# Performance work log

Hardware: AMD Instinct MI355X
Metric: run time of the kernel (lower is better)

## Reference

```python
import jax, jax.numpy as jnp
import numpy as np

LATENT = 128
HEADS = 4
HEAD_DIM = LATENT // HEADS
NUM_BUCKETS = 32
MAX_DISTANCE = 100000
B, N = 8, 2048


def relative_position_bucket(qpos, kpos):
    """T5-style bidirectional relative position bucketing.
    qpos, kpos: [B, N] int -> buckets [B, N, N] int32 in [0, NUM_BUCKETS).
    """
    rel = kpos[:, None, :] - qpos[:, :, None]  # [B, Nq, Nk]
    half = NUM_BUCKETS // 2
    buckets = (rel > 0).astype(jnp.int32) * half
    arel = jnp.abs(rel)
    max_exact = half // 2
    is_small = arel < max_exact
    # log-spaced buckets for larger distances
    large = max_exact + (
        jnp.log(jnp.maximum(arel, 1).astype(jnp.float32) / max_exact)
        / np.log(MAX_DISTANCE / max_exact)
        * (half - max_exact)
    ).astype(jnp.int32)
    large = jnp.minimum(large, half - 1)
    return buckets + jnp.where(is_small, arel.astype(jnp.int32), large)


def setup_inputs() -> dict:
    key = jax.random.key(0)
    ks = jax.random.split(key, 12)
    s = 0.02
    x = jax.random.normal(ks[0], (B, N, LATENT), dtype=jnp.float32)
    positions = jnp.sort(jax.random.randint(ks[1], (B, N), 0, 1000000), axis=-1)
    mask = jnp.ones((B, N), dtype=bool)
    Wq = jax.random.normal(ks[2], (LATENT, LATENT), dtype=jnp.float32) * s
    bq = jax.random.normal(ks[3], (LATENT,), dtype=jnp.float32) * s
    Wk = jax.random.normal(ks[4], (LATENT, LATENT), dtype=jnp.float32) * s
    bk = jax.random.normal(ks[5], (LATENT,), dtype=jnp.float32) * s
    Wv = jax.random.normal(ks[6], (LATENT, LATENT), dtype=jnp.float32) * s
    bv = jax.random.normal(ks[7], (LATENT,), dtype=jnp.float32) * s
    pos_w = jax.random.normal(ks[8], (NUM_BUCKETS + 1, HEADS), dtype=jnp.float32) * s
    Wo = jax.random.normal(ks[9], (LATENT, LATENT), dtype=jnp.float32) * s
    bo = jax.random.normal(ks[10], (LATENT,), dtype=jnp.float32) * s
    return {"x": x, "positions": positions, "mask": mask,
            "Wq": Wq, "bq": bq, "Wk": Wk, "bk": bk, "Wv": Wv, "bv": bv,
            "pos_w": pos_w, "Wo": Wo, "bo": bo}


def reference(x, positions, mask, Wq, bq, Wk, bk, Wv, bv, pos_w, Wo, bo):
    b, n, _ = x.shape
    # QKV projections, split heads: [b, h, n, d]
    Q = (x @ Wq + bq).reshape(b, n, HEADS, HEAD_DIM).transpose(0, 2, 1, 3)
    K = (x @ Wk + bk).reshape(b, n, HEADS, HEAD_DIM).transpose(0, 2, 1, 3)
    V = (x @ Wv + bv).reshape(b, n, HEADS, HEAD_DIM).transpose(0, 2, 1, 3)
    scores = jnp.einsum("bhqd,bhkd->bhqk", Q, K) / jnp.sqrt(
        jnp.asarray(HEAD_DIM, dtype=x.dtype))
    buckets = relative_position_bucket(positions, positions)  # [b, n, n]
    bias = pos_w[buckets]                  # [b, n, n, h]
    scores = scores + bias.transpose(0, 3, 1, 2)  # [b, h, n, n]
    scores = jnp.where(mask[:, None, None, :], scores, -jnp.inf)
    attn = jax.nn.softmax(scores, axis=-1)
    attn = jnp.nan_to_num(attn, nan=0.0)
    attended = jnp.einsum("bhqk,bhkd->bhqd", attn, V)
    attended = attended.transpose(0, 2, 1, 3).reshape(b, n, LATENT)
    return attended @ Wo + bo
```

## Files before the change

### kernel.cpp

```cpp
#include <hip/hip_runtime.h>
#include <math.h>


#define LOG2E 1.4426950408889634f
#define QKV_SCALE 0.17677669529663687f
#define QS (QKV_SCALE * LOG2E)

typedef _Float16 half8 __attribute__((ext_vector_type(8)));
typedef float ffrag __attribute__((ext_vector_type(4)));

#if __has_builtin(__builtin_amdgcn_exp2f)
#define EXP2F __builtin_amdgcn_exp2f
#else
#define EXP2F exp2f
#endif

static __device__ __forceinline__ unsigned short f16bits(float f) {
    return __builtin_bit_cast(unsigned short, (_Float16)f);
}
static __device__ __forceinline__ float h16f(unsigned int bits) {
    return (float)__builtin_bit_cast(_Float16, (unsigned short)(bits & 0xFFFFu));
}
static __device__ __forceinline__ unsigned int pk2(float a, float b) {
    return __builtin_bit_cast(unsigned int, __builtin_amdgcn_cvt_pkrtz(a, b));
}
static __device__ __forceinline__ void async_cp16(const unsigned short* g, unsigned short* l) {
    __builtin_amdgcn_global_load_lds(
        (const __attribute__((address_space(1))) unsigned int*)g,
        (__attribute__((address_space(3))) unsigned int*)l, 16, 0, 0);
}

__device__ __constant__ int SN_TAB[32] = {
     -2000000000,
    -30755, -9458, -2908, -894, -275, -84, -26,
    -7, -6, -5, -4, -3, -2, -1,
    0,
    1, 2, 3, 4, 5, 6, 7,
    8,
    27, 85, 276, 895, 2909, 9459, 30756,
    2000000000 };

__global__ __launch_bounds__(256)
void prep_seg_kernel(const float* __restrict__ Wq, const float* __restrict__ Wk,
                     const float* __restrict__ Wv, const float* __restrict__ Wo,
                     const float* __restrict__ bq, const float* __restrict__ bk,
                     const float* __restrict__ bv,
                     const int* __restrict__ positions,
                     unsigned short* __restrict__ Wt_qkv,
                     unsigned short* __restrict__ Wt_o,
                     float* __restrict__ bias_qkv,
                     unsigned int* __restrict__ segtab)
{
    if (blockIdx.x < 256) {
        const int e = blockIdx.x * 256 + threadIdx.x;
        const int m = e >> 14, r = e & 16383;
        const int c = r >> 7, k = r & 127;
        float v;
        if (m == 0)      v = Wq[k * 128 + c] * QS;
        else if (m == 1) v = Wk[k * 128 + c];
        else if (m == 2) v = Wv[k * 128 + c];
        else             v = Wo[k * 128 + c];
        if (m < 3) Wt_qkv[(m * 128 + c) * 128 + k] = f16bits(v);
        else       Wt_o[c * 128 + k] = f16bits(v);
        if (e < 128)      bias_qkv[e] = bq[e] * QS;
        else if (e < 256) bias_qkv[e] = bk[e - 128];
        else if (e < 384) bias_qkv[e] = bv[e - 256];
        return;
    }
    const int gid = (blockIdx.x - 256) * 256 + threadIdx.x;
    const int row = gid >> 5;
    const int s = gid & 31;
    const int b = row >> 11;
    const int* kp = positions + b * 2048;
    const int qp = kp[row & 2047];
    const int bucket = (s < 15) ? (15 - s) : (s == 15 ? 0 : s + 1);
    if (s == 31) { segtab[row * 32 + s] = (2048u << 16) | 31u; return; }
    const int target = qp + SN_TAB[s + 1];
    int lo = 0, hi = 2048;
    while (lo < hi) { const int mid = (lo + hi) >> 1; if (kp[mid] < target) lo = mid + 1; else hi = mid; }
    segtab[row * 32 + s] = ((unsigned)lo << 16) | (unsigned)bucket;
}

__global__ __launch_bounds__(512)
void qkv_mfma(const float* __restrict__ x, const unsigned short* __restrict__ Wt,
              const float* __restrict__ bias_qkv,
              unsigned short* __restrict__ Qb, unsigned short* __restrict__ Kb,
              unsigned short* __restrict__ Vg2)
{
    __shared__ __align__(16) unsigned short Xs[64 * 136];
    const int tid = threadIdx.x;
    const int token0 = blockIdx.x * 64;
    #pragma unroll
    for (int it = 0; it < 4; ++it) {
        const int f = tid + it * 512;
        const int row = f >> 5, k0 = (f & 31) << 2;
        const float4 xv = *(const float4*)(x + (size_t)(token0 + row) * 128 + k0);
        uint2 u;
        u.x = pk2(xv.x, xv.y);
        u.y = pk2(xv.z, xv.w);
        *(uint2*)(Xs + row * 136 + k0) = u;
    }
    __syncthreads();

    const int wave = tid >> 6, lane = tid & 63;
    const int lq = lane & 15, quad = lane >> 4;
    const int b = token0 >> 11;
    const int n0 = token0 & 2047;

    #pragma unroll
    for (int j = 0; j < 3; ++j) {
        const int ct = wave + j * 8;
        const int colbase = ct * 16;
        half8 wf[4];
        #pragma unroll
        for (int ks = 0; ks < 4; ++ks)
            wf[ks] = *(const half8*)(Wt + (colbase + lq) * 128 + ks * 32 + quad * 8);

        if (ct < 16) {
            const int c0q = colbase + quad * 4;
            const float4 bv = *(const float4*)(bias_qkv + c0q);
            #pragma unroll
            for (int msub = 0; msub < 4; ++msub) {
                ffrag acc = {bv.x, bv.y, bv.z, bv.w};
                #pragma unroll
                for (int ks = 0; ks < 4; ++ks) {
                    const half8 xf = *(const half8*)(Xs + (msub * 16 + lq) * 136 + ks * 32 + quad * 8);
                    acc = __builtin_amdgcn_mfma_f32_16x16x32_f16(wf[ks], xf, acc, 0, 0, 0);
                }
                const int n = n0 + msub * 16 + lq;
                const int c0 = c0q & 127;
                const int h = c0 >> 5, d = c0 & 31;
                const ushort4 v4 = make_ushort4(f16bits(acc[0]), f16bits(acc[1]),
                                                f16bits(acc[2]), f16bits(acc[3]));
                unsigned short* base = (ct < 8) ? Qb : Kb;
                *(ushort4*)(base + ((size_t)(b * 4 + h) * 2048 + n) * 32 + d) = v4;
            }
        } else {
            const float bias = bias_qkv[colbase + lq];
            const int c2 = colbase + lq - 256;
            const int h = c2 >> 5, d = c2 & 31;
            const size_t bhh = (size_t)(b * 4 + h);
            #pragma unroll
            for (int msub = 0; msub < 4; ++msub) {
                ffrag acc = {bias, bias, bias, bias};
                #pragma unroll
                for (int ks = 0; ks < 4; ++ks) {
                    const half8 xf = *(const half8*)(Xs + (msub * 16 + lq) * 136 + ks * 32 + quad * 8);
                    acc = __builtin_amdgcn_mfma_f32_16x16x32_f16(xf, wf[ks], acc, 0, 0, 0);
                }
                const int n = n0 + msub * 16 + quad * 4;
                const int chunk = n >> 7, kloc = n & 127;
                const int win = kloc >> 5, rem = kloc & 31;
                const int half = rem >> 4, pg = (rem >> 2) & 3;
                const int G = d * 16 + ((win * 4 + pg) ^ (d & 15));
                const size_t off = ((bhh * 16 + chunk) * 512 + G) * 8 + half * 4;
                const ushort4 v4 = make_ushort4(f16bits(acc[0]), f16bits(acc[1]),
                                                f16bits(acc[2]), f16bits(acc[3]));
                *(ushort4*)(Vg2 + off) = v4;
            }
        }
    }
}

__global__ __launch_bounds__(512, 4)
void attn_kernel(const unsigned short* __restrict__ Qb,
                 const unsigned short* __restrict__ Kb,
                 const unsigned short* __restrict__ Vg2,
                 const unsigned int* __restrict__ segtab,
                 const float* __restrict__ pos_w,
                 unsigned short* __restrict__ att)
{
    __shared__ __align__(16) unsigned short VB[2][2][4096];
    __shared__ unsigned int Sg[128 * 32];

    const int tid = threadIdx.x;
    const int wave = __builtin_amdgcn_readfirstlane(tid >> 6);
    const int lane = tid & 63;
    const int lq = lane & 15, quad = lane >> 4;
    const int group = wave >> 2, wg = wave & 3;

    const int qt = blockIdx.x & 15;
    const int bh = blockIdx.x >> 4;
    const int b = bh >> 2, h = bh & 3;
    const int q0 = qt * 128;

    const unsigned short* Kg = Kb + (size_t)bh * 2048 * 32;
    const unsigned short* Vgb = Vg2 + (size_t)bh * 65536;

    #pragma unroll
    for (int it = 0; it < 2; ++it) {
        const int g = (wg * 2 + it) * 64 + lane;
        async_cp16(Vgb + (size_t)group * 4096 + g * 8, &VB[group][0][(wg * 2 + it) * 512]);
    }

    {
        const unsigned int* src = segtab + ((size_t)b * 2048 + q0) * 32;
        #pragma unroll
        for (int it = 0; it < 2; ++it) {
            const int e4 = tid + it * 512;
            uint4 u = *(const uint4*)(src + e4 * 4);
            unsigned int* c = &u.x;
            const int row = e4 >> 3, s0 = (e4 & 7) * 4;
            const int rx = row & 31;
            #pragma unroll
            for (int i = 0; i < 4; ++i) {
                const float wf = __expf(pos_w[(c[i] & 0xFFFFu) * 4 + h]);
                Sg[row * 32 + ((s0 + i) ^ rx)] = (c[i] & 0xFFFF0000u) | f16bits(wf);
            }
        }
    }

    const int qa = q0 + wg * 32 + lq;
    const int qbn = qa + 16;
    const half8 qfa = *(const half8*)(Qb + ((size_t)bh * 2048 + qa) * 32 + quad * 8);
    const half8 qfb = *(const half8*)(Qb + ((size_t)bh * 2048 + qbn) * 32 + quad * 8);

    half8 ones;
    #pragma unroll
    for (int i = 0; i < 8; ++i) ones[i] = (_Float16)1.0f;

    ffrag o0a = {0.f,0.f,0.f,0.f}, o1a = {0.f,0.f,0.f,0.f}, o2a = {0.f,0.f,0.f,0.f};
    ffrag o0b = {0.f,0.f,0.f,0.f}, o1b = {0.f,0.f,0.f,0.f}, o2b = {0.f,0.f,0.f,0.f};
    int cura = -1, enda = 0; float wfa = 0.f;
    int curb = -1, endb = 0; float wfb = 0.f;
    const int rowa = wg * 32 + lq, rowb = rowa + 16;
    const int sga = rowa * 32, xa = rowa & 31;
    const int sgb = rowb * 32, xb = rowb & 31;

    half8 kA[4], kB[4];
    {
        const int kc0 = group * 128;
        #pragma unroll
        for (int j = 0; j < 4; ++j)
            kA[j] = *(const half8*)(Kg + (size_t)(kc0 + j * 16 + lq) * 32 + quad * 8);
    }

    __syncthreads();

    auto half_chunk = [&](const half8* karr, const unsigned short* vb, int kc, int w0) {
        #pragma unroll
        for (int dw = 0; dw < 2; ++dw) {
            const int w = w0 + dw;
            unsigned int pua[4], pub[4];
            #pragma unroll
            for (int T = 0; T < 2; ++T) {
                const half8 kf = karr[dw * 2 + T];
                ffrag sa = {0.f,0.f,0.f,0.f}, sb = {0.f,0.f,0.f,0.f};
                sa = __builtin_amdgcn_mfma_f32_16x16x32_f16(kf, qfa, sa, 0, 0, 0);
                sb = __builtin_amdgcn_mfma_f32_16x16x32_f16(kf, qfb, sb, 0, 0, 0);
                const int kidx = kc + (w * 2 + T) * 16 + quad * 4;
                float pa[4], pb[4];
                if (__builtin_expect(__any(kidx + 3 >= enda), 0)) {
                    #pragma unroll
                    for (int r = 0; r < 4; ++r) {
                        while (kidx + r >= enda) {
                            const unsigned int u = Sg[sga + ((++cura) ^ xa)];
                            enda = (int)(u >> 16); wfa = h16f(u);
                        }
                        pa[r] = EXP2F(sa[r]) * wfa;
                    }
                } else {
                    #pragma unroll
                    for (int r = 0; r < 4; ++r) pa[r] = EXP2F(sa[r]) * wfa;
                }
                if (__builtin_expect(__any(kidx + 3 >= endb), 0)) {
                    #pragma unroll
                    for (int r = 0; r < 4; ++r) {
                        while (kidx + r >= endb) {
                            const unsigned int u = Sg[sgb + ((++curb) ^ xb)];
                            endb = (int)(u >> 16); wfb = h16f(u);
                        }
                        pb[r] = EXP2F(sb[r]) * wfb;
                    }
                } else {
                    #pragma unroll
                    for (int r = 0; r < 4; ++r) pb[r] = EXP2F(sb[r]) * wfb;
                }
                pua[T * 2 + 0] = pk2(pa[0], pa[1]);
                pua[T * 2 + 1] = pk2(pa[2], pa[3]);
                pub[T * 2 + 0] = pk2(pb[0], pb[1]);
                pub[T * 2 + 1] = pk2(pb[2], pb[3]);
            }
            const int c = (w * 4 + quad) ^ lq;
            const half8 A0 = *(const half8*)(vb + (lq * 16 + c) * 8);
            const half8 A1 = *(const half8*)(vb + ((16 + lq) * 16 + c) * 8);
            const half8 Ba = __builtin_bit_cast(half8, make_int4(pua[0], pua[1], pua[2], pua[3]));
            const half8 Bb = __builtin_bit_cast(half8, make_int4(pub[0], pub[1], pub[2], pub[3]));
            o0a = __builtin_amdgcn_mfma_f32_16x16x32_f16(A0, Ba, o0a, 0, 0, 0);
            o1a = __builtin_amdgcn_mfma_f32_16x16x32_f16(A1, Ba, o1a, 0, 0, 0);
            o2a = __builtin_amdgcn_mfma_f32_16x16x32_f16(ones, Ba, o2a, 0, 0, 0);
            o0b = __builtin_amdgcn_mfma_f32_16x16x32_f16(A0, Bb, o0b, 0, 0, 0);
            o1b = __builtin_amdgcn_mfma_f32_16x16x32_f16(A1, Bb, o1b, 0, 0, 0);
            o2b = __builtin_amdgcn_mfma_f32_16x16x32_f16(ones, Bb, o2b, 0, 0, 0);
        }
    };

    for (int i = 0; i < 8; ++i) {
        const int kc = (2 * i + group) * 128;
        const unsigned short* vb = &VB[group][i & 1][0];
        if (i < 7) {
            #pragma unroll
            for (int it = 0; it < 2; ++it) {
                const int g = (wg * 2 + it) * 64 + lane;
                async_cp16(Vgb + (size_t)(2 * i + group + 2) * 4096 + g * 8,
                           &VB[group][(i + 1) & 1][(wg * 2 + it) * 512]);
            }
        }
        #pragma unroll
        for (int j = 0; j < 4; ++j)
            kB[j] = *(const half8*)(Kg + (size_t)(kc + (4 + j) * 16 + lq) * 32 + quad * 8);

        half_chunk(kA, vb, kc, 0);

        const int kcn = (i < 7) ? kc + 256 : kc;
        #pragma unroll
        for (int j = 0; j < 4; ++j)
            kA[j] = *(const half8*)(Kg + (size_t)(kcn + j * 16 + lq) * 32 + quad * 8);

        half_chunk(kB, vb, kc, 2);
        __syncthreads();
    }

    float lsa = o2a[0], lsb = o2b[0];
    float* scr = (float*)&VB[0][0][0];
    if (group == 1) {
        float* s = scr + (wg * 64 + lane) * 18;
        #pragma unroll
        for (int j = 0; j < 4; ++j) {
            s[j] = o0a[j]; s[4 + j] = o1a[j]; s[8 + j] = o0b[j]; s[12 + j] = o1b[j];
        }
        s[16] = lsa; s[17] = lsb;
    }
    __syncthreads();
    if (group == 0) {
        const float* s = scr + (wg * 64 + lane) * 18;
        #pragma unroll
        for (int j = 0; j < 4; ++j) {
            o0a[j] += s[j]; o1a[j] += s[4 + j]; o0b[j] += s[8 + j]; o1b[j] += s[12 + j];
        }
        lsa += s[16]; lsb += s[17];
        const float inva = 1.0f / lsa;
        const float invb = 1.0f / lsb;

        unsigned short* da = att + (size_t)(b * 2048 + qa) * 128 + h * 32 + quad * 4;
        uint2 r0, r1;
        r0.x = pk2(o0a[0] * inva, o0a[1] * inva);
        r0.y = pk2(o0a[2] * inva, o0a[3] * inva);
        r1.x = pk2(o1a[0] * inva, o1a[1] * inva);
        r1.y = pk2(o1a[2] * inva, o1a[3] * inva);
        *(uint2*)da = r0;
        *(uint2*)(da + 16) = r1;

        unsigned short* db = att + (size_t)(b * 2048 + qbn) * 128 + h * 32 + quad * 4;
        r0.x = pk2(o0b[0] * invb, o0b[1] * invb);
        r0.y = pk2(o0b[2] * invb, o0b[3] * invb);
        r1.x = pk2(o1b[0] * invb, o1b[1] * invb);
        r1.y = pk2(o1b[2] * invb, o1b[3] * invb);
        *(uint2*)db = r0;
        *(uint2*)(db + 16) = r1;
    }
}

__global__ __launch_bounds__(512)
void out_mfma(const unsigned short* __restrict__ att,
              const unsigned short* __restrict__ Wt_o,
              const float* __restrict__ bo, float* __restrict__ out)
{
    __shared__ __align__(16) unsigned short Xs[64 * 136];
    const int tid = threadIdx.x;
    const int token0 = blockIdx.x * 64;
    #pragma unroll
    for (int it = 0; it < 2; ++it) {
        const int f = tid + it * 512;
        const int row = f >> 4, k0 = (f & 15) << 3;
        const uint4 v = *(const uint4*)(att + (size_t)(token0 + row) * 128 + k0);
        *(uint4*)(Xs + row * 136 + k0) = v;
    }
    __syncthreads();

    const int wave = tid >> 6, lane = tid & 63;
    const int lq = lane & 15, quad = lane >> 4;
    const int colbase = wave * 16;

    half8 wf[4];
    #pragma unroll
    for (int ks = 0; ks < 4; ++ks)
        wf[ks] = *(const half8*)(Wt_o + (colbase + lq) * 128 + ks * 32 + quad * 8);
    const float4 bv = *(const float4*)(bo + colbase + quad * 4);

    #pragma unroll
    for (int msub = 0; msub < 4; ++msub) {
        ffrag acc = {bv.x, bv.y, bv.z, bv.w};
        #pragma unroll
        for (int ks = 0; ks < 4; ++ks) {
            const half8 xf = *(const half8*)(Xs + (msub * 16 + lq) * 136 + ks * 32 + quad * 8);
            acc = __builtin_amdgcn_mfma_f32_16x16x32_f16(wf[ks], xf, acc, 0, 0, 0);
        }
        const int c0 = colbase + quad * 4;
        *(float4*)(out + (size_t)(token0 + msub * 16 + lq) * 128 + c0) =
            make_float4(acc[0], acc[1], acc[2], acc[3]);
    }
}

extern "C" void kernel_launch(void* const* d_in, const int* in_sizes, int n_in,
                              void* d_out, int out_size, void* d_ws, size_t ws_size,
                              hipStream_t stream)
{
    const float* x         = (const float*)d_in[0];
    const int*   positions = (const int*)d_in[1];
    const float* Wq = (const float*)d_in[3];
    const float* bq = (const float*)d_in[4];
    const float* Wk = (const float*)d_in[5];
    const float* bk = (const float*)d_in[6];
    const float* Wv = (const float*)d_in[7];
    const float* bv = (const float*)d_in[8];
    const float* pw = (const float*)d_in[9];
    const float* Wo = (const float*)d_in[10];
    const float* bo = (const float*)d_in[11];
    float* out = (float*)d_out;

    unsigned short* Qb  = (unsigned short*)d_ws;
    unsigned short* Kb  = Qb + 2097152;
    unsigned short* Vg2 = Kb + 2097152;
    unsigned short* att = Vg2 + 2097152;
    unsigned int* segtab = (unsigned int*)(att + 2097152);
    unsigned short* Wt_qkv = (unsigned short*)(segtab + 524288);
    unsigned short* Wt_o = Wt_qkv + 49152;
    float* bias_qkv = (float*)(Wt_o + 16384);

    prep_seg_kernel<<<2304, 256, 0, stream>>>(Wq, Wk, Wv, Wo, bq, bk, bv, positions,
                                              Wt_qkv, Wt_o, bias_qkv, segtab);
    qkv_mfma<<<256, 512, 0, stream>>>(x, Wt_qkv, bias_qkv, Qb, Kb, Vg2);
    attn_kernel<<<512, 512, 0, stream>>>(Qb, Kb, Vg2, segtab, pw, att);
    out_mfma<<<256, 512, 0, stream>>>(att, Wt_o, bo, out);
}
```

Measured before the change: 149.2 us.

## Drop LDS staging: register-resident projections and direct-global K/V loads in attention

The QKV and output projection kernels now use small 128-thread blocks over 16 tokens that load activations straight into MFMA register fragments, with no shared-memory staging. Biases are read directly rather than from a precomputed buffer. The attention kernel drops the async global-to-LDS double-buffered V copies and reads V fragments directly from global memory in a new unswizzled layout, interleaving K/V loads with compute. The aim is to remove LDS traffic and barriers, at the cost of relying on cache and latency hiding for the global loads.

```diff
diff --git a/kernel.cpp b/kernel.cpp
--- a/kernel.cpp
+++ b/kernel.cpp
@@ -24,14 +24,9 @@
 static __device__ __forceinline__ unsigned int pk2(float a, float b) {
     return __builtin_bit_cast(unsigned int, __builtin_amdgcn_cvt_pkrtz(a, b));
 }
-static __device__ __forceinline__ void async_cp16(const unsigned short* g, unsigned short* l) {
-    __builtin_amdgcn_global_load_lds(
-        (const __attribute__((address_space(1))) unsigned int*)g,
-        (__attribute__((address_space(3))) unsigned int*)l, 16, 0, 0);
-}
 
 __device__ __constant__ int SN_TAB[32] = {
-     -2000000000,
+    -2000000000,
     -30755, -9458, -2908, -894, -275, -84, -26,
     -7, -6, -5, -4, -3, -2, -1,
     0,
@@ -41,15 +36,12 @@
     2000000000 };
 
 __global__ __launch_bounds__(256)
-void prep_seg_kernel(const float* __restrict__ Wq, const float* __restrict__ Wk,
-                     const float* __restrict__ Wv, const float* __restrict__ Wo,
-                     const float* __restrict__ bq, const float* __restrict__ bk,
-                     const float* __restrict__ bv,
-                     const int* __restrict__ positions,
-                     unsigned short* __restrict__ Wt_qkv,
-                     unsigned short* __restrict__ Wt_o,
-                     float* __restrict__ bias_qkv,
-                     unsigned int* __restrict__ segtab)
+void pre_seg_kernel(const float* __restrict__ Wq, const float* __restrict__ Wk,
+                    const float* __restrict__ Wv, const float* __restrict__ Wo,
+                    const int* __restrict__ positions,
+                    unsigned short* __restrict__ Wt_qkv,
+                    unsigned short* __restrict__ Wt_o,
+                    unsigned int* __restrict__ segtab)
 {
     if (blockIdx.x < 256) {
         const int e = blockIdx.x * 256 + threadIdx.x;
@@ -62,9 +54,6 @@
         else             v = Wo[k * 128 + c];
         if (m < 3) Wt_qkv[(m * 128 + c) * 128 + k] = f16bits(v);
         else       Wt_o[c * 128 + k] = f16bits(v);
-        if (e < 128)      bias_qkv[e] = bq[e] * QS;
-        else if (e < 256) bias_qkv[e] = bk[e - 128];
-        else if (e < 384) bias_qkv[e] = bv[e - 256];
         return;
     }
     const int gid = (blockIdx.x - 256) * 256 + threadIdx.x;
@@ -81,84 +70,81 @@
     segtab[row * 32 + s] = ((unsigned)lo << 16) | (unsigned)bucket;
 }
 
-__global__ __launch_bounds__(512)
-void qkv_mfma(const float* __restrict__ x, const unsigned short* __restrict__ Wt,
-              const float* __restrict__ bias_qkv,
-              unsigned short* __restrict__ Qb, unsigned short* __restrict__ Kb,
-              unsigned short* __restrict__ Vg2)
+__global__ __launch_bounds__(128)
+void qkv_reg(const float* __restrict__ x, const unsigned short* __restrict__ Wt,
+             const float* __restrict__ bq, const float* __restrict__ bk,
+             const float* __restrict__ bv,
+             unsigned short* __restrict__ Qb, unsigned short* __restrict__ Kb,
+             unsigned short* __restrict__ Vg2)
 {
-    __shared__ __align__(16) unsigned short Xs[64 * 136];
     const int tid = threadIdx.x;
-    const int token0 = blockIdx.x * 64;
-    #pragma unroll
-    for (int it = 0; it < 4; ++it) {
-        const int f = tid + it * 512;
-        const int row = f >> 5, k0 = (f & 31) << 2;
-        const float4 xv = *(const float4*)(x + (size_t)(token0 + row) * 128 + k0);
-        uint2 u;
-        u.x = pk2(xv.x, xv.y);
-        u.y = pk2(xv.z, xv.w);
-        *(uint2*)(Xs + row * 136 + k0) = u;
-    }
-    __syncthreads();
-
     const int wave = tid >> 6, lane = tid & 63;
     const int lq = lane & 15, quad = lane >> 4;
+    const int token0 = blockIdx.x * 16;
     const int b = token0 >> 11;
     const int n0 = token0 & 2047;
 
-    #pragma unroll
-    for (int j = 0; j < 3; ++j) {
-        const int ct = wave + j * 8;
+    half8 xf[4];
+    #pragma unroll
+    for (int ks = 0; ks < 4; ++ks) {
+        const float* xp = x + (size_t)(token0 + lq) * 128 + ks * 32 + quad * 8;
+        const float4 a = *(const float4*)xp;
+        const float4 c = *(const float4*)(xp + 4);
+        xf[ks] = __builtin_bit_cast(half8,
+                 make_int4(pk2(a.x, a.y), pk2(a.z, a.w), pk2(c.x, c.y), pk2(c.z, c.w)));
+    }
+
+    #pragma unroll
+    for (int jj = 0; jj < 8; ++jj) {
+        const int ct = wave * 8 + jj;
         const int colbase = ct * 16;
         half8 wf[4];
         #pragma unroll
         for (int ks = 0; ks < 4; ++ks)
-            wf[ks] = *(const half8*)(Wt + (colbase + lq) * 128 + ks * 32 + quad * 8);
-
-        if (ct < 16) {
-            const int c0q = colbase + quad * 4;
-            const float4 bv = *(const float4*)(bias_qkv + c0q);
-            #pragma unroll
-            for (int msub = 0; msub < 4; ++msub) {
-                ffrag acc = {bv.x, bv.y, bv.z, bv.w};
-                #pragma unroll
-                for (int ks = 0; ks < 4; ++ks) {
-                    const half8 xf = *(const half8*)(Xs + (msub * 16 + lq) * 136 + ks * 32 + quad * 8);
-                    acc = __builtin_amdgcn_mfma_f32_16x16x32_f16(wf[ks], xf, acc, 0, 0, 0);
-                }
-                const int n = n0 + msub * 16 + lq;
-                const int c0 = c0q & 127;
-                const int h = c0 >> 5, d = c0 & 31;
-                const ushort4 v4 = make_ushort4(f16bits(acc[0]), f16bits(acc[1]),
-                                                f16bits(acc[2]), f16bits(acc[3]));
-                unsigned short* base = (ct < 8) ? Qb : Kb;
-                *(ushort4*)(base + ((size_t)(b * 4 + h) * 2048 + n) * 32 + d) = v4;
-            }
+            wf[ks] = *(const half8*)(Wt + (size_t)(colbase + lq) * 128 + ks * 32 + quad * 8);
+        const int c0 = colbase + quad * 4;
+        const int cl = (ct < 8) ? c0 : (c0 - 128);
+        float4 bias;
+        if (ct < 8) {
+            bias = *(const float4*)(bq + c0);
+            bias.x *= QS; bias.y *= QS; bias.z *= QS; bias.w *= QS;
         } else {
-            const float bias = bias_qkv[colbase + lq];
-            const int c2 = colbase + lq - 256;
-            const int h = c2 >> 5, d = c2 & 31;
-            const size_t bhh = (size_t)(b * 4 + h);
-            #pragma unroll
-            for (int msub = 0; msub < 4; ++msub) {
-                ffrag acc = {bias, bias, bias, bias};
-                #pragma unroll
-                for (int ks = 0; ks < 4; ++ks) {
-                    const half8 xf = *(const half8*)(Xs + (msub * 16 + lq) * 136 + ks * 32 + quad * 8);
-                    acc = __builtin_amdgcn_mfma_f32_16x16x32_f16(xf, wf[ks], acc, 0, 0, 0);
-                }
-                const int n = n0 + msub * 16 + quad * 4;
-                const int chunk = n >> 7, kloc = n & 127;
-                const int win = kloc >> 5, rem = kloc & 31;
-                const int half = rem >> 4, pg = (rem >> 2) & 3;
-                const int G = d * 16 + ((win * 4 + pg) ^ (d & 15));
-                const size_t off = ((bhh * 16 + chunk) * 512 + G) * 8 + half * 4;
-                const ushort4 v4 = make_ushort4(f16bits(acc[0]), f16bits(acc[1]),
-                                                f16bits(acc[2]), f16bits(acc[3]));
-                *(ushort4*)(Vg2 + off) = v4;
-            }
+            bias = *(const float4*)(bk + cl);
         }
+        ffrag acc = {bias.x, bias.y, bias.z, bias.w};
+        #pragma unroll
+        for (int ks = 0; ks < 4; ++ks)
+            acc = __builtin_amdgcn_mfma_f32_16x16x32_f16(wf[ks], xf[ks], acc, 0, 0, 0);
+        const int h = cl >> 5, d = cl & 31;
+        const ushort4 v4 = make_ushort4(f16bits(acc[0]), f16bits(acc[1]),
+                                        f16bits(acc[2]), f16bits(acc[3]));
+        unsigned short* base = (ct < 8) ? Qb : Kb;
+        *(ushort4*)(base + ((size_t)(b * 4 + h) * 2048 + n0 + lq) * 32 + d) = v4;
+    }
+
+    #pragma unroll
+    for (int jj = 0; jj < 4; ++jj) {
+        const int ct = 16 + wave * 4 + jj;
+        const int colbase = ct * 16;
+        half8 wf[4];
+        #pragma unroll
+        for (int ks = 0; ks < 4; ++ks)
+            wf[ks] = *(const half8*)(Wt + (size_t)(colbase + lq) * 128 + ks * 32 + quad * 8);
+        const int col128 = colbase + lq - 256;
+        const float bias = bv[col128];
+        ffrag acc = {bias, bias, bias, bias};
+        #pragma unroll
+        for (int ks = 0; ks < 4; ++ks)
+            acc = __builtin_amdgcn_mfma_f32_16x16x32_f16(xf[ks], wf[ks], acc, 0, 0, 0);
+        const int h = col128 >> 5, d = col128 & 31;
+        const int nn = n0 + quad * 4;
+        const int chunk = nn >> 7, kloc = nn & 127;
+        const int win = kloc >> 5, rem = kloc & 31;
+        const int hlf = rem >> 4, pg = (rem >> 2) & 3;
+        const size_t off = (((size_t)(b * 4 + h) * 16 + chunk) * 512
+                            + win * 128 + d * 4 + pg) * 8 + hlf * 4;
+        *(ushort4*)(Vg2 + off) = make_ushort4(f16bits(acc[0]), f16bits(acc[1]),
+                                              f16bits(acc[2]), f16bits(acc[3]));
     }
 }
 
@@ -170,28 +156,21 @@
                  const float* __restrict__ pos_w,
                  unsigned short* __restrict__ att)
 {
-    __shared__ __align__(16) unsigned short VB[2][2][4096];
-    __shared__ unsigned int Sg[128 * 32];
+    __shared__ __align__(16) unsigned int SMEM[4672];
+    unsigned int* Sg = SMEM;
 
     const int tid = threadIdx.x;
     const int wave = __builtin_amdgcn_readfirstlane(tid >> 6);
     const int lane = tid & 63;
     const int lq = lane & 15, quad = lane >> 4;
-    const int group = wave >> 2, wg = wave & 3;
-
-    const int qt = blockIdx.x & 15;
-    const int bh = blockIdx.x >> 4;
+    const int g = wave >> 2, wg = wave & 3;
+
+    const int qt = blockIdx.x & 15, bh = blockIdx.x >> 4;
     const int b = bh >> 2, h = bh & 3;
     const int q0 = qt * 128;
 
-    const unsigned short* Kg = Kb + (size_t)bh * 2048 * 32;
+    const unsigned short* Kg = Kb + (size_t)bh * 65536;
     const unsigned short* Vgb = Vg2 + (size_t)bh * 65536;
-
-    #pragma unroll
-    for (int it = 0; it < 2; ++it) {
-        const int g = (wg * 2 + it) * 64 + lane;
-        async_cp16(Vgb + (size_t)group * 4096 + g * 8, &VB[group][0][(wg * 2 + it) * 512]);
-    }
 
     {
         const unsigned int* src = segtab + ((size_t)b * 2048 + q0) * 32;
@@ -203,9 +182,9 @@
             const int row = e4 >> 3, s0 = (e4 & 7) * 4;
             const int rx = row & 31;
             #pragma unroll
-            for (int i = 0; i < 4; ++i) {
-                const float wf = __expf(pos_w[(c[i] & 0xFFFFu) * 4 + h]);
-                Sg[row * 32 + ((s0 + i) ^ rx)] = (c[i] & 0xFFFF0000u) | f16bits(wf);
+            for (int i2 = 0; i2 < 4; ++i2) {
+                const float wfv = __expf(pos_w[(c[i2] & 0xFFFFu) * 4 + h]);
+                Sg[row * 32 + ((s0 + i2) ^ rx)] = (c[i2] & 0xFFFF0000u) | f16bits(wfv);
             }
         }
     }
@@ -227,28 +206,34 @@
     const int sga = rowa * 32, xa = rowa & 31;
     const int sgb = rowb * 32, xb = rowb & 31;
 
-    half8 kA[4], kB[4];
-    {
-        const int kc0 = group * 128;
+    half8 kf[2][4], vf[4];
+    const int gv = (lq * 4 + quad) * 8;
+
+    auto load_k = [&](half8* dst, int idx) {
+        const int kb0 = idx * 64;
         #pragma unroll
         for (int j = 0; j < 4; ++j)
-            kA[j] = *(const half8*)(Kg + (size_t)(kc0 + j * 16 + lq) * 32 + quad * 8);
-    }
-
-    __syncthreads();
-
-    auto half_chunk = [&](const half8* karr, const unsigned short* vb, int kc, int w0) {
+            dst[j] = *(const half8*)(Kg + (size_t)(kb0 + j * 16 + lq) * 32 + quad * 8);
+    };
+    auto load_v = [&](int idx) {
+        const unsigned short* vp = Vgb + (size_t)(idx >> 1) * 4096 + (idx & 1) * 2048 + gv;
+        vf[0] = *(const half8*)(vp);
+        vf[1] = *(const half8*)(vp + 512);
+        vf[2] = *(const half8*)(vp + 1024);
+        vf[3] = *(const half8*)(vp + 1536);
+    };
+    auto compute = [&](const half8* karr, int idx) {
+        const int kb0 = idx * 64;
         #pragma unroll
         for (int dw = 0; dw < 2; ++dw) {
-            const int w = w0 + dw;
             unsigned int pua[4], pub[4];
             #pragma unroll
             for (int T = 0; T < 2; ++T) {
-                const half8 kf = karr[dw * 2 + T];
+                const half8 kfc = karr[dw * 2 + T];
                 ffrag sa = {0.f,0.f,0.f,0.f}, sb = {0.f,0.f,0.f,0.f};
-                sa = __builtin_amdgcn_mfma_f32_16x16x32_f16(kf, qfa, sa, 0, 0, 0);
-                sb = __builtin_amdgcn_mfma_f32_16x16x32_f16(kf, qfb, sb, 0, 0, 0);
-                const int kidx = kc + (w * 2 + T) * 16 + quad * 4;
+                sa = __builtin_amdgcn_mfma_f32_16x16x32_f16(kfc, qfa, sa, 0, 0, 0);
+                sb = __builtin_amdgcn_mfma_f32_16x16x32_f16(kfc, qfb, sb, 0, 0, 0);
+                const int kidx = kb0 + dw * 32 + T * 16 + quad * 4;
                 float pa[4], pb[4];
                 if (__builtin_expect(__any(kidx + 3 >= enda), 0)) {
                     #pragma unroll
@@ -281,9 +266,8 @@
                 pub[T * 2 + 0] = pk2(pb[0], pb[1]);
                 pub[T * 2 + 1] = pk2(pb[2], pb[3]);
             }
-            const int c = (w * 4 + quad) ^ lq;
-            const half8 A0 = *(const half8*)(vb + (lq * 16 + c) * 8);
-            const half8 A1 = *(const half8*)(vb + ((16 + lq) * 16 + c) * 8);
+            const half8 A0 = vf[dw * 2];
+            const half8 A1 = vf[dw * 2 + 1];
             const half8 Ba = __builtin_bit_cast(half8, make_int4(pua[0], pua[1], pua[2], pua[3]));
             const half8 Bb = __builtin_bit_cast(half8, make_int4(pub[0], pub[1], pub[2], pub[3]));
             o0a = __builtin_amdgcn_mfma_f32_16x16x32_f16(A0, Ba, o0a, 0, 0, 0);
@@ -295,35 +279,24 @@
         }
     };
 
+    __syncthreads();
+    load_k(kf[0], g * 2);
+
+    #pragma unroll 1
     for (int i = 0; i < 8; ++i) {
-        const int kc = (2 * i + group) * 128;
-        const unsigned short* vb = &VB[group][i & 1][0];
-        if (i < 7) {
-            #pragma unroll
-            for (int it = 0; it < 2; ++it) {
-                const int g = (wg * 2 + it) * 64 + lane;
-                async_cp16(Vgb + (size_t)(2 * i + group + 2) * 4096 + g * 8,
-                           &VB[group][(i + 1) & 1][(wg * 2 + it) * 512]);
-            }
-        }
-        #pragma unroll
-        for (int j = 0; j < 4; ++j)
-            kB[j] = *(const half8*)(Kg + (size_t)(kc + (4 + j) * 16 + lq) * 32 + quad * 8);
-
-        half_chunk(kA, vb, kc, 0);
-
-        const int kcn = (i < 7) ? kc + 256 : kc;
-        #pragma unroll
-        for (int j = 0; j < 4; ++j)
-            kA[j] = *(const half8*)(Kg + (size_t)(kcn + j * 16 + lq) * 32 + quad * 8);
-
-        half_chunk(kB, vb, kc, 2);
-        __syncthreads();
+        const int ci = 2 * i + g;
+        load_v(ci * 2);
+        load_k(kf[1], ci * 2 + 1);
+        compute(kf[0], ci * 2);
+        load_v(ci * 2 + 1);
+        if (i < 7) load_k(kf[0], ci * 2 + 4);
+        compute(kf[1], ci * 2 + 1);
     }
 
     float lsa = o2a[0], lsb = o2b[0];
-    float* scr = (float*)&VB[0][0][0];
-    if (group == 1) {
+    __syncthreads();
+    float* scr = (float*)SMEM;
+    if (g == 1) {
         float* s = scr + (wg * 64 + lane) * 18;
         #pragma unroll
         for (int j = 0; j < 4; ++j) {
@@ -332,7 +305,7 @@
         s[16] = lsa; s[17] = lsb;
     }
     __syncthreads();
-    if (group == 0) {
+    if (g == 0) {
         const float* s = scr + (wg * 64 + lane) * 18;
         #pragma unroll
         for (int j = 0; j < 4; ++j) {
@@ -361,43 +334,36 @@
     }
 }
 
-__global__ __launch_bounds__(512)
-void out_mfma(const unsigned short* __restrict__ att,
-              const unsigned short* __restrict__ Wt_o,
-              const float* __restrict__ bo, float* __restrict__ out)
+__global__ __launch_bounds__(128)
+void out_reg(const unsigned short* __restrict__ att,
+             const unsigned short* __restrict__ Wt_o,
+             const float* __restrict__ bo, float* __restrict__ out)
 {
-    __shared__ __align__(16) unsigned short Xs[64 * 136];
     const int tid = threadIdx.x;
-    const int token0 = blockIdx.x * 64;
-    #pragma unroll
-    for (int it = 0; it < 2; ++it) {
-        const int f = tid + it * 512;
-        const int row = f >> 4, k0 = (f & 15) << 3;
-        const uint4 v = *(const uint4*)(att + (size_t)(token0 + row) * 128 + k0);
-        *(uint4*)(Xs + row * 136 + k0) = v;
-    }
-    __syncthreads();
-
     const int wave = tid >> 6, lane = tid & 63;
     const int lq = lane & 15, quad = lane >> 4;
-    const int colbase = wave * 16;
-
-    half8 wf[4];
+    const int token0 = blockIdx.x * 16;
+
+    half8 af[4];
     #pragma unroll
     for (int ks = 0; ks < 4; ++ks)
-        wf[ks] = *(const half8*)(Wt_o + (colbase + lq) * 128 + ks * 32 + quad * 8);
-    const float4 bv = *(const float4*)(bo + colbase + quad * 4);
-
-    #pragma unroll
-    for (int msub = 0; msub < 4; ++msub) {
-        ffrag acc = {bv.x, bv.y, bv.z, bv.w};
-        #pragma unroll
-        for (int ks = 0; ks < 4; ++ks) {
-            const half8 xf = *(const half8*)(Xs + (msub * 16 + lq) * 136 + ks * 32 + quad * 8);
-            acc = __builtin_amdgcn_mfma_f32_16x16x32_f16(wf[ks], xf, acc, 0, 0, 0);
-        }
+        af[ks] = *(const half8*)(att + (size_t)(token0 + lq) * 128 + ks * 32 + quad * 8);
+
+    #pragma unroll
+    for (int jj = 0; jj < 4; ++jj) {
+        const int ct = wave * 4 + jj;
+        const int colbase = ct * 16;
+        half8 wf[4];
+        #pragma unroll
+        for (int ks = 0; ks < 4; ++ks)
+            wf[ks] = *(const half8*)(Wt_o + (size_t)(colbase + lq) * 128 + ks * 32 + quad * 8);
         const int c0 = colbase + quad * 4;
-        *(float4*)(out + (size_t)(token0 + msub * 16 + lq) * 128 + c0) =
+        const float4 bias = *(const float4*)(bo + c0);
+        ffrag acc = {bias.x, bias.y, bias.z, bias.w};
+        #pragma unroll
+        for (int ks = 0; ks < 4; ++ks)
+            acc = __builtin_amdgcn_mfma_f32_16x16x32_f16(wf[ks], af[ks], acc, 0, 0, 0);
+        *(float4*)(out + (size_t)(token0 + lq) * 128 + c0) =
             make_float4(acc[0], acc[1], acc[2], acc[3]);
     }
 }
@@ -426,11 +392,10 @@
     unsigned int* segtab = (unsigned int*)(att + 2097152);
     unsigned short* Wt_qkv = (unsigned short*)(segtab + 524288);
     unsigned short* Wt_o = Wt_qkv + 49152;
-    float* bias_qkv = (float*)(Wt_o + 16384);
-
-    prep_seg_kernel<<<2304, 256, 0, stream>>>(Wq, Wk, Wv, Wo, bq, bk, bv, positions,
-                                              Wt_qkv, Wt_o, bias_qkv, segtab);
-    qkv_mfma<<<256, 512, 0, stream>>>(x, Wt_qkv, bias_qkv, Qb, Kb, Vg2);
+
+    pre_seg_kernel<<<2304, 256, 0, stream>>>(Wq, Wk, Wv, Wo, positions,
+                                             Wt_qkv, Wt_o, segtab);
+    qkv_reg<<<1024, 128, 0, stream>>>(x, Wt_qkv, bq, bk, bv, Qb, Kb, Vg2);
     attn_kernel<<<512, 512, 0, stream>>>(Qb, Kb, Vg2, segtab, pw, att);
-    out_mfma<<<256, 512, 0, stream>>>(att, Wt_o, bo, out);
-}
+    out_reg<<<1024, 128, 0, stream>>>(att, Wt_o, bo, out);
+}
```

Measured after the change: 161.1 us. +8.0%, slower.
